# Kernel tuning notes

Measured on AMD Instinct MI355X. Metric: run time of the kernel, lower is better.

Reference implementation:

```python
import jax, jax.numpy as jnp
import numpy as np

B, S, NU, ML, H, V = 32, 256, 4, 9, 768, 30522


def setup_inputs() -> dict:
    key = jax.random.key(0)
    ks = jax.random.split(key, 13)
    s = 1.0 / np.sqrt(H)
    return {
        "x": jax.random.randint(ks[0], (B, S), 0, V),
        "decoder_input": jax.random.normal(ks[1], (B, NU, H), jnp.float32) * 0.02,
        "encoder_output": jax.random.normal(ks[2], (B, S, H), jnp.float32) * 0.02,
        "hidden": jax.random.normal(ks[3], (1, B, H), jnp.float32) * 0.02,
        "max_len": ML,
        "teacher": jax.random.randint(ks[4], (B, NU, ML), 0, V),
        "embed_w": jax.random.normal(ks[5], (V, H), jnp.float32) * 0.02,
        "gru_w_ih": jax.random.uniform(ks[6], (3 * H, H), jnp.float32, -s, s),
        "gru_w_hh": jax.random.uniform(ks[7], (3 * H, H), jnp.float32, -s, s),
        "gru_b_ih": jax.random.uniform(ks[8], (3 * H,), jnp.float32, -s, s),
        "gru_b_hh": jax.random.uniform(ks[9], (3 * H,), jnp.float32, -s, s),
        "w_gen_w": jax.random.uniform(ks[10], (1, 3 * H), jnp.float32, -s, s),
        "w_gen_b": jax.random.uniform(ks[11], (1,), jnp.float32, -s, s),
    }


def reference(x, decoder_input, encoder_output, hidden, max_len, teacher,
              embed_w, gru_w_ih, gru_w_hh, gru_b_ih, gru_b_hh, w_gen_w, w_gen_b):
    pad_mask = (x == 0)                       # [B, S]
    b, nu, h_dim = decoder_input.shape
    h0 = hidden[0]                            # [B, H]

    # Teacher-forced input sequence for every (update, step): [NU*ML, B, H]
    tf = embed_w[teacher[:, :, :max_len - 1]]           # [B, NU, ML-1, H]
    tf = jnp.moveaxis(tf, 0, 2)                          # [NU, ML-1, B, H]
    first = jnp.swapaxes(decoder_input, 0, 1)[:, None]   # [NU, 1, B, H]
    ws = jnp.concatenate([first, tf], axis=1).reshape(nu * max_len, b, h_dim)

    def gru_cell(w, h):
        gi = w @ gru_w_ih.T + gru_b_ih        # [B, 3H]
        gh = h @ gru_w_hh.T + gru_b_hh
        i_r, i_z, i_n = jnp.split(gi, 3, axis=-1)
        h_r, h_z, h_n = jnp.split(gh, 3, axis=-1)
        r = jax.nn.sigmoid(i_r + h_r)
        z = jax.nn.sigmoid(i_z + h_z)
        n = jnp.tanh(i_n + r * h_n)
        return (1.0 - z) * n + z * h

    batch_idx = jnp.arange(b)[:, None]

    def step(h, w):
        h = gru_cell(w, h)                                    # [B, H]
        attn_e = jnp.einsum('bsh,bh->bs', encoder_output, h)  # [B, S]
        attn_e = jnp.where(pad_mask, -1e9, attn_e)
        attn_history = jax.nn.softmax(attn_e, axis=-1)        # [B, S]
        attn_vocab = jax.nn.softmax(h @ embed_w.T, axis=-1)   # [B, V]
        context = jnp.einsum('bs,bsh->bh', attn_history, encoder_output)
        gate_in = jnp.concatenate([w, h, context], axis=-1)   # [B, 3H]
        p_gen = jax.nn.sigmoid(gate_in @ w_gen_w.T + w_gen_b) # [B, 1]
        p_ctx = jnp.zeros_like(attn_vocab).at[batch_idx, x].add(attn_history)
        p_final = p_gen * attn_vocab + (1.0 - p_gen) * p_ctx  # [B, V]
        return h, p_final

    _, outs = jax.lax.scan(step, h0, ws)          # [NU*ML, B, V]
    outs = outs.reshape(nu, max_len, b, -1)       # [NU, ML, B, V]
    return jnp.transpose(outs, (2, 0, 1, 3))      # [B, NU, ML, V]
```

## Files before the change

### kernel.cpp

```cpp
#include <hip/hip_runtime.h>
#include <math.h>

#define BB_ 32
#define SS_ 256
#define HH_ 768
#define VV_ 30522
#define TT_ 36
#define MM_ 1152
#define NBLK_GRU 48

typedef __bf16 bf16x8 __attribute__((ext_vector_type(8)));
typedef __bf16 bf16x4 __attribute__((ext_vector_type(4)));
typedef float f32x4 __attribute__((ext_vector_type(4)));

__device__ __forceinline__ float sigmoidf_(float x) { return 1.f / (1.f + expf(-x)); }

__device__ __forceinline__ void async_load16(const void* g, void* l) {
  __builtin_amdgcn_global_load_lds(
      (const __attribute__((address_space(1))) void*)g,
      (__attribute__((address_space(3))) void*)l, 16, 0, 0);
}

__global__ __launch_bounds__(256) void cvt_bf16(const float* __restrict__ s,
                                                __bf16* __restrict__ d, int n4) {
  int i = blockIdx.x * 256 + threadIdx.x;
  if (i < n4) {
    float4 v = reinterpret_cast<const float4*>(s)[i];
    bf16x4 o;
    o[0] = (__bf16)v.x; o[1] = (__bf16)v.y; o[2] = (__bf16)v.z; o[3] = (__bf16)v.w;
    reinterpret_cast<bf16x4*>(d)[i] = o;
  }
}

__global__ __launch_bounds__(256) void build_ws(const float* __restrict__ dec,
                                                const int* __restrict__ teacher,
                                                const float* __restrict__ embed,
                                                __bf16* __restrict__ wsbf) {
  int idx = blockIdx.x * 256 + threadIdx.x;
  if (idx >= MM_ * HH_) return;
  int m = idx / HH_, k = idx - m * HH_;
  int tau = m >> 5, b = m & 31;
  int u = tau / 9, tt = tau - u * 9;
  float v;
  if (tt == 0) v = dec[((size_t)b * 4 + u) * HH_ + k];
  else v = embed[(size_t)teacher[(b * 4 + u) * 9 + tt - 1] * HH_ + k];
  wsbf[idx] = (__bf16)v;
}

__global__ __launch_bounds__(256) void enc_gate(const float* __restrict__ enc,
                                                const float* __restrict__ wgen,
                                                float* __restrict__ encg) {
  int row = blockIdx.x * 4 + (threadIdx.x >> 6);
  int lane = threadIdx.x & 63;
  const float* er = enc + (size_t)row * HH_;
  float ssum = 0.f;
#pragma unroll
  for (int i = 0; i < 12; ++i) ssum += er[i * 64 + lane] * wgen[1536 + i * 64 + lane];
  for (int off = 32; off; off >>= 1) ssum += __shfl_down(ssum, off);
  if (lane == 0) encg[row] = ssum;
}

template <int MODE>
__global__ __launch_bounds__(256) void gemm_bt2(const __bf16* __restrict__ A,
                                                const __bf16* __restrict__ Bm,
                                                float* __restrict__ C,
                                                float* __restrict__ rowsum,
                                                int Nreal, int ldC) {
  __shared__ __bf16 As[128 * 32];
  __shared__ __bf16 Bs[128 * 32];
  const int tid = threadIdx.x;
  const int lane = tid & 63, wave = tid >> 6;
  const int wm = wave >> 1, wn = wave & 1;
  const int q = lane >> 4, ln = lane & 15;
  const int m0 = blockIdx.y * 128, n0 = blockIdx.x * 128;
  const int srow = (wave << 5) + (lane >> 2);
  const int kc = lane & 3;
  const size_t aoff = (size_t)(m0 + srow) * HH_ + kc * 8;
  const size_t aoff2 = aoff + 16 * HH_;
  int br1 = n0 + srow;      if (br1 >= Nreal) br1 = Nreal - 1;
  int br2 = n0 + srow + 16; if (br2 >= Nreal) br2 = Nreal - 1;
  __bf16* lA1 = &As[srow * 32 + kc * 8];
  __bf16* lA2 = &As[(srow + 16) * 32 + kc * 8];
  __bf16* lB1 = &Bs[srow * 32 + kc * 8];
  __bf16* lB2 = &Bs[(srow + 16) * 32 + kc * 8];
  f32x4 acc[4][4] = {};
  for (int kb = 0; kb < 24; ++kb) {
    const int k0 = kb << 5;
    async_load16(A + aoff + k0, lA1);
    async_load16(A + aoff2 + k0, lA2);
    async_load16(Bm + (size_t)br1 * HH_ + kc * 8 + k0, lB1);
    async_load16(Bm + (size_t)br2 * HH_ + kc * 8 + k0, lB2);
    __syncthreads();
    bf16x8 af[4], bfr[4];
#pragma unroll
    for (int mi = 0; mi < 4; ++mi)
      af[mi] = *reinterpret_cast<const bf16x8*>(&As[(wm * 64 + mi * 16 + ln) * 32 + q * 8]);
#pragma unroll
    for (int ni = 0; ni < 4; ++ni)
      bfr[ni] = *reinterpret_cast<const bf16x8*>(&Bs[(wn * 64 + ni * 16 + ln) * 32 + q * 8]);
#pragma unroll
    for (int mi = 0; mi < 4; ++mi)
#pragma unroll
      for (int ni = 0; ni < 4; ++ni)
        acc[mi][ni] = __builtin_amdgcn_mfma_f32_16x16x32_bf16(af[mi], bfr[ni], acc[mi][ni], 0, 0, 0);
    __syncthreads();
  }
#pragma unroll
  for (int mi = 0; mi < 4; ++mi)
#pragma unroll
    for (int r2 = 0; r2 < 4; ++r2) {
      const int m = m0 + wm * 64 + mi * 16 + q * 4 + r2;
      if (MODE == 0) {
#pragma unroll
        for (int ni = 0; ni < 4; ++ni) {
          int n = n0 + wn * 64 + ni * 16 + ln;
          if (n < Nreal) C[(size_t)m * ldC + n] = acc[mi][ni][r2];
        }
      } else {
        float part = 0.f;
#pragma unroll
        for (int ni = 0; ni < 4; ++ni) {
          int n = n0 + wn * 64 + ni * 16 + ln;
          float e = expf(fminf(acc[mi][ni][r2], 60.f));
          if (n < Nreal) { C[(size_t)m * ldC + n] = e; part += e; }
        }
#pragma unroll
        for (int o = 1; o < 16; o <<= 1) part += __shfl_xor(part, o);
        if (ln == 0) atomicAdd(rowsum + m, part);
      }
    }
}

__global__ __launch_bounds__(128, 1) void gru_scan(const __bf16* __restrict__ hid_bf,
                                                   const float* __restrict__ H0,
                                                   const __bf16* __restrict__ Whh,
                                                   const float* __restrict__ GI,
                                                   const float* __restrict__ bih,
                                                   const float* __restrict__ bhh,
                                                   __bf16* __restrict__ Ah,
                                                   __bf16* __restrict__ Hx,
                                                   unsigned* __restrict__ ctr) {
  __shared__ __bf16 WhhS[48 * HH_];
  const int tid = threadIdx.x, lane = tid & 63;
  const int mi = tid >> 6;
  const int q = lane >> 4, ln = lane & 15;
  const int jH = blockIdx.x * 16 + ln;
  for (int i = tid; i < 48 * 96; i += 128) {
    int row = i / 96, cs = i - row * 96;
    int g = row >> 4, jl = row & 15;
    bf16x8 v = *reinterpret_cast<const bf16x8*>(
        &Whh[((size_t)(g * 768 + blockIdx.x * 16 + jl)) * HH_ + cs * 8]);
    *reinterpret_cast<bf16x8*>(&WhhS[row * HH_ + ((cs ^ (row & 7)) * 8)]) = v;
  }
  const float bir = bih[jH], biz = bih[jH + 768], bin_ = bih[jH + 1536];
  const float bhr = bhh[jH], bhz = bhh[jH + 768], bhn = bhh[jH + 1536];
  float hc[4];
#pragma unroll
  for (int r2 = 0; r2 < 4; ++r2)
    hc[r2] = H0[(size_t)(mi * 16 + q * 4 + r2) * HH_ + jH];
  const __bf16* w0 = &WhhS[(0 + ln) * HH_];
  const __bf16* w1 = &WhhS[(16 + ln) * HH_];
  const __bf16* w2 = &WhhS[(32 + ln) * HH_];
  const int swz = (ln & 7) * 8;
  float gir[4], giz[4], gin[4];
#pragma unroll
  for (int r2 = 0; r2 < 4; ++r2) {
    const float* gi = GI + (size_t)(mi * 16 + q * 4 + r2) * 2304;
    gir[r2] = gi[jH]; giz[r2] = gi[jH + 768]; gin[r2] = gi[jH + 1536];
  }
  __syncthreads();
  for (int tau = 0; tau < TT_; ++tau) {
    const __bf16* arow = tau ? (Hx + (size_t)(((tau - 1) & 1) * 32 + mi * 16 + ln) * HH_)
                             : (hid_bf + (size_t)(mi * 16 + ln) * HH_);
    bf16x8 areg[24];
#pragma unroll
    for (int kb = 0; kb < 24; ++kb)
      areg[kb] = *reinterpret_cast<const bf16x8*>(arow + kb * 32 + q * 8);
    f32x4 a0 = {}, a1 = {}, a2 = {};
#pragma unroll
    for (int kb = 0; kb < 24; ++kb) {
      int kl = (kb * 32 + q * 8) ^ swz;
      bf16x8 b0 = *reinterpret_cast<const bf16x8*>(w0 + kl);
      bf16x8 b1 = *reinterpret_cast<const bf16x8*>(w1 + kl);
      bf16x8 b2 = *reinterpret_cast<const bf16x8*>(w2 + kl);
      a0 = __builtin_amdgcn_mfma_f32_16x16x32_bf16(areg[kb], b0, a0, 0, 0, 0);
      a1 = __builtin_amdgcn_mfma_f32_16x16x32_bf16(areg[kb], b1, a1, 0, 0, 0);
      a2 = __builtin_amdgcn_mfma_f32_16x16x32_bf16(areg[kb], b2, a2, 0, 0, 0);
    }
    __bf16* hxc = Hx + (size_t)((tau & 1) * 32) * HH_;
#pragma unroll
    for (int r2 = 0; r2 < 4; ++r2) {
      int b = mi * 16 + q * 4 + r2;
      float r = sigmoidf_(gir[r2] + bir + a0[r2] + bhr);
      float z = sigmoidf_(giz[r2] + biz + a1[r2] + bhz);
      float n = tanhf(gin[r2] + bin_ + r * (a2[r2] + bhn));
      float h = (1.f - z) * n + z * hc[r2];
      hc[r2] = h;
      float hp = __shfl_xor(h, 1);
      __bf16 hb = (__bf16)h, hpb = (__bf16)hp;
      unsigned lo = (unsigned)__builtin_bit_cast(unsigned short, hb);
      unsigned hi = (unsigned)__builtin_bit_cast(unsigned short, hpb);
      if (!(ln & 1)) {
        unsigned u = lo | (hi << 16);
        *reinterpret_cast<unsigned*>(&Ah[((size_t)b * TT_ + tau) * HH_ + jH]) = u;
        if (tau < TT_ - 1)
          __hip_atomic_store(reinterpret_cast<unsigned*>(&hxc[(size_t)b * HH_ + jH]), u,
                             __ATOMIC_RELAXED, __HIP_MEMORY_SCOPE_AGENT);
      }
    }
    if (tau < TT_ - 1) {
      __syncthreads();
      if (tid == 0)
        __hip_atomic_fetch_add(ctr, 1u, __ATOMIC_RELAXED, __HIP_MEMORY_SCOPE_AGENT);
      {
        const float* GIt = GI + (size_t)(tau + 1) * BB_ * 2304;
#pragma unroll
        for (int r2 = 0; r2 < 4; ++r2) {
          const float* gi = GIt + (size_t)(mi * 16 + q * 4 + r2) * 2304;
          gir[r2] = gi[jH]; giz[r2] = gi[jH + 768]; gin[r2] = gi[jH + 1536];
        }
      }
      if (mi == 0) {
        const unsigned tgt = (unsigned)(tau + 1) * NBLK_GRU;
        int spin = 0;
        while (__hip_atomic_load(ctr, __ATOMIC_RELAXED, __HIP_MEMORY_SCOPE_AGENT) < tgt) {
          __builtin_amdgcn_s_sleep(1);
          if (++spin > (1 << 20)) break;
        }
      }
      __syncthreads();
      __builtin_amdgcn_fence(__ATOMIC_ACQUIRE, "agent");
    }
  }
}

__global__ __launch_bounds__(256) void attn_gemm(const __bf16* __restrict__ Ah,
                                                 const __bf16* __restrict__ encb,
                                                 float* __restrict__ E) {
  int b = blockIdx.x >> 2, stile = blockIdx.x & 3;
  int wave = threadIdx.x >> 6, lane = threadIdx.x & 63;
  int q = lane >> 4, ln = lane & 15;
  int s = stile * 64 + wave * 16 + ln;
  const __bf16* brow = encb + ((size_t)b * SS_ + s) * HH_;
  const __bf16* arow[3];
#pragma unroll
  for (int mt = 0; mt < 3; ++mt) {
    int tau = mt * 16 + ln; if (tau > 35) tau = 35;
    arow[mt] = Ah + ((size_t)b * TT_ + tau) * HH_;
  }
  f32x4 acc[3] = {};
#pragma unroll 4
  for (int kb = 0; kb < 24; ++kb) {
    int k0 = kb * 32 + q * 8;
    bf16x8 bb = *reinterpret_cast<const bf16x8*>(brow + k0);
#pragma unroll
    for (int mt = 0; mt < 3; ++mt) {
      bf16x8 aa = *reinterpret_cast<const bf16x8*>(arow[mt] + k0);
      acc[mt] = __builtin_amdgcn_mfma_f32_16x16x32_bf16(aa, bb, acc[mt], 0, 0, 0);
    }
  }
#pragma unroll
  for (int mt = 0; mt < 3; ++mt)
#pragma unroll
    for (int r2 = 0; r2 < 4; ++r2) {
      int tau = mt * 16 + q * 4 + r2;
      if (tau < 36) E[((size_t)b * TT_ + tau) * SS_ + s] = acc[mt][r2];
    }
}

__global__ __launch_bounds__(256) void softmax_pg(const float* __restrict__ E,
                                                  const int* __restrict__ x,
                                                  const float* __restrict__ encg,
                                                  const __bf16* __restrict__ wsbf,
                                                  const __bf16* __restrict__ Ah,
                                                  const float* __restrict__ wgen,
                                                  const float* __restrict__ wgenb,
                                                  float* __restrict__ attn,
                                                  float* __restrict__ pg) {
  int m = blockIdx.x;
  int b = m / TT_, tau = m - b * TT_;
  int m_in = tau * 32 + b;
  int t = threadIdx.x;
  __shared__ float red[256];
  __shared__ float r1[256], r2[256], r3[256];
  float e = E[(size_t)m * SS_ + t];
  if (x[b * SS_ + t] == 0) e = -1000000000.0f;
  red[t] = e; __syncthreads();
  for (int off = 128; off; off >>= 1) {
    if (t < off) red[t] = fmaxf(red[t], red[t + off]);
    __syncthreads();
  }
  float mx = red[0];
  float p = expf(e - mx);
  float dsum = 0.f;
#pragma unroll
  for (int i = 0; i < 3; ++i) {
    int k = t + i * 256;
    dsum += (float)wsbf[(size_t)m_in * HH_ + k] * wgen[k];
    dsum += (float)Ah[(size_t)m * HH_ + k] * wgen[768 + k];
  }
  float pe = p * encg[b * SS_ + t];
  r1[t] = p; r2[t] = pe; r3[t] = dsum; __syncthreads();
  for (int off = 128; off; off >>= 1) {
    if (t < off) { r1[t] += r1[t + off]; r2[t] += r2[t + off]; r3[t] += r3[t + off]; }
    __syncthreads();
  }
  float Z = r1[0];
  attn[(size_t)m * SS_ + t] = p / Z;
  if (t == 0) pg[m] = sigmoidf_(r3[0] + r2[0] / Z + wgenb[0]);
}

__global__ __launch_bounds__(256) void finalize(float* __restrict__ C,
                                                const float* __restrict__ rowsum,
                                                const float* __restrict__ pg) {
  int m = blockIdx.y;
  float scale = pg[m] / rowsum[m];
  int base_i = blockIdx.x * 2048;
  size_t rowb = (size_t)m * VV_;
#pragma unroll
  for (int j = 0; j < 8; ++j) {
    int i = base_i + j * 256 + threadIdx.x;
    if (i < VV_) C[rowb + i] *= scale;
  }
}

__global__ __launch_bounds__(256) void scatter_ctx(float* __restrict__ C,
                                                   const float* __restrict__ attn,
                                                   const float* __restrict__ pg,
                                                   const int* __restrict__ x) {
  int m = blockIdx.x, s = threadIdx.x;
  int b = m / TT_;
  float v = (1.f - pg[m]) * attn[(size_t)m * SS_ + s];
  int col = x[b * SS_ + s];
  atomicAdd(C + (size_t)m * VV_ + col, v);
}

extern "C" void kernel_launch(void* const* d_in, const int* in_sizes, int n_in,
                              void* d_out, int out_size, void* d_ws, size_t ws_size,
                              hipStream_t stream) {
  const int*   x       = (const int*)d_in[0];
  const float* dec     = (const float*)d_in[1];
  const float* enc     = (const float*)d_in[2];
  const float* hidden  = (const float*)d_in[3];
  const int*   teacher = (const int*)d_in[5];
  const float* embed   = (const float*)d_in[6];
  const float* wih     = (const float*)d_in[7];
  const float* whh     = (const float*)d_in[8];
  const float* bih     = (const float*)d_in[9];
  const float* bhh     = (const float*)d_in[10];
  const float* wgen    = (const float*)d_in[11];
  const float* wgenb   = (const float*)d_in[12];
  float* out = (float*)d_out;

  char* w = (char*)d_ws;
  __bf16* embed_bf = (__bf16*)w;  w += (size_t)VV_ * HH_ * 2;
  __bf16* enc_bf   = (__bf16*)w;  w += (size_t)BB_ * SS_ * HH_ * 2;
  __bf16* wih_bf   = (__bf16*)w;  w += (size_t)2304 * HH_ * 2;
  __bf16* whh_bf   = (__bf16*)w;  w += (size_t)2304 * HH_ * 2;
  __bf16* ws_bf    = (__bf16*)w;  w += (size_t)MM_ * HH_ * 2;
  __bf16* hid_bf   = (__bf16*)w;  w += (size_t)BB_ * HH_ * 2;
  __bf16* A_h      = (__bf16*)w;  w += (size_t)MM_ * HH_ * 2;
  float*  GI       = (float*)w;   w += (size_t)MM_ * 2304 * 4;
  float*  E        = (float*)w;   w += (size_t)MM_ * SS_ * 4;
  float*  attn     = (float*)w;   w += (size_t)MM_ * SS_ * 4;
  float*  encg     = (float*)w;   w += (size_t)BB_ * SS_ * 4;
  float*  pg       = (float*)w;   w += 8192;
  char*   ctl      = w;           w += 8192;
  __bf16* Hx       = (__bf16*)w;  w += (size_t)2 * BB_ * HH_ * 2;
  float*    rowsum = (float*)ctl;
  unsigned* ctr    = (unsigned*)(ctl + 4864);

  hipMemsetAsync(ctl, 0, 8192, stream);

  cvt_bf16<<<(VV_ * HH_ / 4 + 255) / 256, 256, 0, stream>>>(embed, embed_bf, VV_ * HH_ / 4);
  cvt_bf16<<<(BB_ * SS_ * HH_ / 4 + 255) / 256, 256, 0, stream>>>(enc, enc_bf, BB_ * SS_ * HH_ / 4);
  cvt_bf16<<<(2304 * HH_ / 4 + 255) / 256, 256, 0, stream>>>(wih, wih_bf, 2304 * HH_ / 4);
  cvt_bf16<<<(2304 * HH_ / 4 + 255) / 256, 256, 0, stream>>>(whh, whh_bf, 2304 * HH_ / 4);
  cvt_bf16<<<(BB_ * HH_ / 4 + 255) / 256, 256, 0, stream>>>(hidden, hid_bf, BB_ * HH_ / 4);

  build_ws<<<(MM_ * HH_ + 255) / 256, 256, 0, stream>>>(dec, teacher, embed, ws_bf);

  gemm_bt2<0><<<dim3(2304 / 128, MM_ / 128), 256, 0, stream>>>(ws_bf, wih_bf, GI, nullptr, 2304, 2304);

  enc_gate<<<BB_ * SS_ / 4, 256, 0, stream>>>(enc, wgen, encg);

  gru_scan<<<NBLK_GRU, 128, 0, stream>>>(hid_bf, hidden, whh_bf, GI, bih, bhh, A_h, Hx, ctr);

  attn_gemm<<<BB_ * 4, 256, 0, stream>>>(A_h, enc_bf, E);
  softmax_pg<<<MM_, 256, 0, stream>>>(E, x, encg, ws_bf, A_h, wgen, wgenb, attn, pg);

  gemm_bt2<1><<<dim3((VV_ + 127) / 128, MM_ / 128), 256, 0, stream>>>(A_h, embed_bf, out, rowsum, VV_, VV_);

  finalize<<<dim3((VV_ + 2047) / 2048, MM_), 256, 0, stream>>>(out, rowsum, pg);
  scatter_ctx<<<MM_, 256, 0, stream>>>(out, attn, pg, x);
}
```

Baseline: 789.9 us.

## Replace GRU grid barrier with step-tagged hidden-state polling

The persistent GRU scan no longer uses a global atomic counter barrier between timesteps. Each hidden value is now stored as a 32-bit word that packs the bf16 value with the step tag. Consumers spin on cache-bypassing loads until every word they need carries the expected tag, then repack the values into bf16 for the MFMA. This removes the counter round-trip and the two block syncs per step. In exchange the hidden-state buffer is twice as large, a memset is added, and correctness relies on sc1 load/store visibility and the ordering of the tags.

```diff
diff --git a/kernel.cpp b/kernel.cpp
--- a/kernel.cpp
+++ b/kernel.cpp
@@ -12,6 +12,7 @@
 typedef __bf16 bf16x8 __attribute__((ext_vector_type(8)));
 typedef __bf16 bf16x4 __attribute__((ext_vector_type(4)));
 typedef float f32x4 __attribute__((ext_vector_type(4)));
+typedef unsigned int u32x4 __attribute__((ext_vector_type(4)));
 
 __device__ __forceinline__ float sigmoidf_(float x) { return 1.f / (1.f + expf(-x)); }
 
@@ -131,6 +132,10 @@
     }
 }
 
+#define LDX(I, OFF) \
+  asm volatile("global_load_dwordx4 %0, %1, off offset:" OFF " sc1" \
+               : "=v"(raw[I]) : "v"(ab) : "memory")
+
 __global__ __launch_bounds__(128, 1) void gru_scan(const __bf16* __restrict__ hid_bf,
                                                    const float* __restrict__ H0,
                                                    const __bf16* __restrict__ Whh,
@@ -138,8 +143,7 @@
                                                    const float* __restrict__ bih,
                                                    const float* __restrict__ bhh,
                                                    __bf16* __restrict__ Ah,
-                                                   __bf16* __restrict__ Hx,
-                                                   unsigned* __restrict__ ctr) {
+                                                   unsigned* __restrict__ Hx2) {
   __shared__ __bf16 WhhS[48 * HH_];
   const int tid = threadIdx.x, lane = tid & 63;
   const int mi = tid >> 6;
@@ -170,24 +174,70 @@
   }
   __syncthreads();
   for (int tau = 0; tau < TT_; ++tau) {
-    const __bf16* arow = tau ? (Hx + (size_t)(((tau - 1) & 1) * 32 + mi * 16 + ln) * HH_)
-                             : (hid_bf + (size_t)(mi * 16 + ln) * HH_);
-    bf16x8 areg[24];
-#pragma unroll
-    for (int kb = 0; kb < 24; ++kb)
-      areg[kb] = *reinterpret_cast<const bf16x8*>(arow + kb * 32 + q * 8);
     f32x4 a0 = {}, a1 = {}, a2 = {};
-#pragma unroll
-    for (int kb = 0; kb < 24; ++kb) {
-      int kl = (kb * 32 + q * 8) ^ swz;
-      bf16x8 b0 = *reinterpret_cast<const bf16x8*>(w0 + kl);
-      bf16x8 b1 = *reinterpret_cast<const bf16x8*>(w1 + kl);
-      bf16x8 b2 = *reinterpret_cast<const bf16x8*>(w2 + kl);
-      a0 = __builtin_amdgcn_mfma_f32_16x16x32_bf16(areg[kb], b0, a0, 0, 0, 0);
-      a1 = __builtin_amdgcn_mfma_f32_16x16x32_bf16(areg[kb], b1, a1, 0, 0, 0);
-      a2 = __builtin_amdgcn_mfma_f32_16x16x32_bf16(areg[kb], b2, a2, 0, 0, 0);
-    }
-    __bf16* hxc = Hx + (size_t)((tau & 1) * 32) * HH_;
+    if (tau == 0) {
+      const __bf16* arow = hid_bf + (size_t)(mi * 16 + ln) * HH_;
+      bf16x8 areg[24];
+#pragma unroll
+      for (int kb = 0; kb < 24; ++kb)
+        areg[kb] = *reinterpret_cast<const bf16x8*>(arow + kb * 32 + q * 8);
+#pragma unroll
+      for (int kb = 0; kb < 24; ++kb) {
+        int kl = (kb * 32 + q * 8) ^ swz;
+        bf16x8 b0 = *reinterpret_cast<const bf16x8*>(w0 + kl);
+        bf16x8 b1 = *reinterpret_cast<const bf16x8*>(w1 + kl);
+        bf16x8 b2 = *reinterpret_cast<const bf16x8*>(w2 + kl);
+        a0 = __builtin_amdgcn_mfma_f32_16x16x32_bf16(areg[kb], b0, a0, 0, 0, 0);
+        a1 = __builtin_amdgcn_mfma_f32_16x16x32_bf16(areg[kb], b1, a1, 0, 0, 0);
+        a2 = __builtin_amdgcn_mfma_f32_16x16x32_bf16(areg[kb], b2, a2, 0, 0, 0);
+      }
+    } else {
+      const unsigned* ab = Hx2 + ((size_t)(((tau - 1) & 1) * 32 + mi * 16 + ln)) * HH_ + q * 8;
+      const unsigned tag = (unsigned)tau;
+      u32x4 raw[48];
+      int spin = 0;
+      while (true) {
+        LDX(0, "0");    LDX(1, "16");   LDX(2, "128");  LDX(3, "144");
+        LDX(4, "256");  LDX(5, "272");  LDX(6, "384");  LDX(7, "400");
+        LDX(8, "512");  LDX(9, "528");  LDX(10, "640"); LDX(11, "656");
+        LDX(12, "768"); LDX(13, "784"); LDX(14, "896"); LDX(15, "912");
+        LDX(16, "1024"); LDX(17, "1040"); LDX(18, "1152"); LDX(19, "1168");
+        LDX(20, "1280"); LDX(21, "1296"); LDX(22, "1408"); LDX(23, "1424");
+        LDX(24, "1536"); LDX(25, "1552"); LDX(26, "1664"); LDX(27, "1680");
+        LDX(28, "1792"); LDX(29, "1808"); LDX(30, "1920"); LDX(31, "1936");
+        LDX(32, "2048"); LDX(33, "2064"); LDX(34, "2176"); LDX(35, "2192");
+        LDX(36, "2304"); LDX(37, "2320"); LDX(38, "2432"); LDX(39, "2448");
+        LDX(40, "2560"); LDX(41, "2576"); LDX(42, "2688"); LDX(43, "2704");
+        LDX(44, "2816"); LDX(45, "2832"); LDX(46, "2944"); LDX(47, "2960");
+        asm volatile("s_waitcnt vmcnt(0)" ::: "memory");
+        __builtin_amdgcn_sched_barrier(0);
+        int ok = 1;
+#pragma unroll
+        for (int i = 0; i < 48; ++i)
+#pragma unroll
+          for (int j = 0; j < 4; ++j) ok &= ((raw[i][j] >> 16) == tag);
+        if (__all(ok)) break;
+        if (++spin > 16384) break;
+        __builtin_amdgcn_s_sleep(1);
+      }
+#pragma unroll
+      for (int kb = 0; kb < 24; ++kb) {
+        u32x4 lo = raw[2 * kb], hi = raw[2 * kb + 1];
+        u32x4 pk;
+        pk[0] = __builtin_amdgcn_perm(lo[1], lo[0], 0x05040100);
+        pk[1] = __builtin_amdgcn_perm(lo[3], lo[2], 0x05040100);
+        pk[2] = __builtin_amdgcn_perm(hi[1], hi[0], 0x05040100);
+        pk[3] = __builtin_amdgcn_perm(hi[3], hi[2], 0x05040100);
+        bf16x8 a = __builtin_bit_cast(bf16x8, pk);
+        int kl = (kb * 32 + q * 8) ^ swz;
+        bf16x8 b0 = *reinterpret_cast<const bf16x8*>(w0 + kl);
+        bf16x8 b1 = *reinterpret_cast<const bf16x8*>(w1 + kl);
+        bf16x8 b2 = *reinterpret_cast<const bf16x8*>(w2 + kl);
+        a0 = __builtin_amdgcn_mfma_f32_16x16x32_bf16(a, b0, a0, 0, 0, 0);
+        a1 = __builtin_amdgcn_mfma_f32_16x16x32_bf16(a, b1, a1, 0, 0, 0);
+        a2 = __builtin_amdgcn_mfma_f32_16x16x32_bf16(a, b2, a2, 0, 0, 0);
+      }
+    }
 #pragma unroll
     for (int r2 = 0; r2 < 4; ++r2) {
       int b = mi * 16 + q * 4 + r2;
@@ -196,40 +246,29 @@
       float n = tanhf(gin[r2] + bin_ + r * (a2[r2] + bhn));
       float h = (1.f - z) * n + z * hc[r2];
       hc[r2] = h;
+      __bf16 hb = (__bf16)h;
+      if (tau < TT_ - 1) {
+        unsigned tv = ((unsigned)(tau + 1) << 16) |
+                      (unsigned)__builtin_bit_cast(unsigned short, hb);
+        unsigned* hx = Hx2 + ((size_t)(((tau & 1) * 32) + b)) * HH_ + jH;
+        asm volatile("global_store_dword %0, %1, off sc1" :: "v"(hx), "v"(tv) : "memory");
+      }
       float hp = __shfl_xor(h, 1);
-      __bf16 hb = (__bf16)h, hpb = (__bf16)hp;
+      __bf16 hpb = (__bf16)hp;
       unsigned lo = (unsigned)__builtin_bit_cast(unsigned short, hb);
       unsigned hi = (unsigned)__builtin_bit_cast(unsigned short, hpb);
       if (!(ln & 1)) {
         unsigned u = lo | (hi << 16);
         *reinterpret_cast<unsigned*>(&Ah[((size_t)b * TT_ + tau) * HH_ + jH]) = u;
-        if (tau < TT_ - 1)
-          __hip_atomic_store(reinterpret_cast<unsigned*>(&hxc[(size_t)b * HH_ + jH]), u,
-                             __ATOMIC_RELAXED, __HIP_MEMORY_SCOPE_AGENT);
       }
     }
     if (tau < TT_ - 1) {
-      __syncthreads();
-      if (tid == 0)
-        __hip_atomic_fetch_add(ctr, 1u, __ATOMIC_RELAXED, __HIP_MEMORY_SCOPE_AGENT);
-      {
-        const float* GIt = GI + (size_t)(tau + 1) * BB_ * 2304;
-#pragma unroll
-        for (int r2 = 0; r2 < 4; ++r2) {
-          const float* gi = GIt + (size_t)(mi * 16 + q * 4 + r2) * 2304;
-          gir[r2] = gi[jH]; giz[r2] = gi[jH + 768]; gin[r2] = gi[jH + 1536];
-        }
-      }
-      if (mi == 0) {
-        const unsigned tgt = (unsigned)(tau + 1) * NBLK_GRU;
-        int spin = 0;
-        while (__hip_atomic_load(ctr, __ATOMIC_RELAXED, __HIP_MEMORY_SCOPE_AGENT) < tgt) {
-          __builtin_amdgcn_s_sleep(1);
-          if (++spin > (1 << 20)) break;
-        }
-      }
-      __syncthreads();
-      __builtin_amdgcn_fence(__ATOMIC_ACQUIRE, "agent");
+      const float* GIt = GI + (size_t)(tau + 1) * BB_ * 2304;
+#pragma unroll
+      for (int r2 = 0; r2 < 4; ++r2) {
+        const float* gi = GIt + (size_t)(mi * 16 + q * 4 + r2) * 2304;
+        gir[r2] = gi[jH]; giz[r2] = gi[jH + 768]; gin[r2] = gi[jH + 1536];
+      }
     }
   }
 }
@@ -366,11 +405,11 @@
   float*  encg     = (float*)w;   w += (size_t)BB_ * SS_ * 4;
   float*  pg       = (float*)w;   w += 8192;
   char*   ctl      = w;           w += 8192;
-  __bf16* Hx       = (__bf16*)w;  w += (size_t)2 * BB_ * HH_ * 2;
+  unsigned* Hx2    = (unsigned*)w; w += (size_t)2 * BB_ * HH_ * 4;
   float*    rowsum = (float*)ctl;
-  unsigned* ctr    = (unsigned*)(ctl + 4864);
 
   hipMemsetAsync(ctl, 0, 8192, stream);
+  hipMemsetAsync(Hx2, 0, (size_t)2 * BB_ * HH_ * 4, stream);
 
   cvt_bf16<<<(VV_ * HH_ / 4 + 255) / 256, 256, 0, stream>>>(embed, embed_bf, VV_ * HH_ / 4);
   cvt_bf16<<<(BB_ * SS_ * HH_ / 4 + 255) / 256, 256, 0, stream>>>(enc, enc_bf, BB_ * SS_ * HH_ / 4);
@@ -384,7 +423,7 @@
 
   enc_gate<<<BB_ * SS_ / 4, 256, 0, stream>>>(enc, wgen, encg);
 
-  gru_scan<<<NBLK_GRU, 128, 0, stream>>>(hid_bf, hidden, whh_bf, GI, bih, bhh, A_h, Hx, ctr);
+  gru_scan<<<NBLK_GRU, 128, 0, stream>>>(hid_bf, hidden, whh_bf, GI, bih, bhh, A_h, Hx2);
 
   attn_gemm<<<BB_ * 4, 256, 0, stream>>>(A_h, enc_bf, E);
   softmax_pg<<<MM_, 256, 0, stream>>>(E, x, encg, ws_bf, A_h, wgen, wgenb, attn, pg);
```

After: 915.5 us. +15.9%, slower.
